# Kernel tuning notes

Hardware: AMD Instinct MI355X
Metric: run time of the kernel (lower is better)

## Reference

```python
import jax, jax.numpy as jnp
import numpy as np

D = 1024        # embedding_dim
H = 16          # num_heads
HKV = 4         # num_kv_heads
HD = D // H     # head_dim = 64
L = 64          # latent_dim
EPS = 1e-6
LN_EPS = 1e-5
B, S = 2, 1024


def _feat(x):
    # feature_map == 'elu': elu(x) + 1 (non-negative features)
    return jax.nn.elu(x) + 1.0


def setup_inputs() -> dict:
    key = jax.random.key(0)
    ks = jax.random.split(key, 8)
    w = lambda k, shape: (jax.random.normal(k, shape, jnp.float32) * 0.02)
    return {
        "x": jax.random.normal(ks[0], (B, S, D), jnp.float32),
        "Wq": w(ks[1], (D, D)), "bq": jnp.zeros((D,), jnp.float32),
        "Wk": w(ks[2], (D, HKV * HD)), "bk": jnp.zeros((HKV * HD,), jnp.float32),
        "Wv": w(ks[3], (D, HKV * HD)), "bv": jnp.zeros((HKV * HD,), jnp.float32),
        "Wc": w(ks[4], (HKV * HD, L)),   # kv_compress (no bias)
        "We": w(ks[5], (L, HKV * HD)),   # kv_expand (no bias)
        "Wo": w(ks[6], (D, D)), "bo": jnp.zeros((D,), jnp.float32),
        "gamma": jnp.ones((D,), jnp.float32),
        "beta": jnp.zeros((D,), jnp.float32),
    }


def reference(x, Wq, bq, Wk, bk, Wv, bv, Wc, We, Wo, bo, gamma, beta):
    b, s, _ = x.shape
    residual = x
    # projections
    q = x @ Wq + bq                     # [b,s,D]
    k = x @ Wk + bk                     # [b,s,HKV*HD]
    v = x @ Wv + bv
    # latent compress -> expand
    k = (k @ Wc) @ We                   # [b,s,HKV*HD]
    v = (v @ Wc) @ We
    # split heads
    q = q.reshape(b, s, H, HD).transpose(0, 2, 1, 3)      # [b,H,s,HD]
    k = k.reshape(b, s, HKV, HD).transpose(0, 2, 1, 3)    # [b,HKV,s,HD]
    v = v.reshape(b, s, HKV, HD).transpose(0, 2, 1, 3)
    # GQA: repeat KV heads per query group
    rep = H // HKV
    k = jnp.repeat(k, rep, axis=1)                        # [b,H,s,HD]
    v = jnp.repeat(v, rep, axis=1)
    # causal linear attention via cumulative KV outer-product state
    qf = _feat(q)                                          # [b,h,s,f]
    kf = _feat(k)
    kv = jnp.einsum('bhsf,bhsd->bhsfd', kf, v)             # [b,h,s,f,d]
    kv_cum = jnp.cumsum(kv, axis=2)
    num = jnp.einsum('bhsf,bhsfd->bhsd', qf, kv_cum)
    den = jnp.einsum('bhsf,bhsf->bhs', qf, jnp.cumsum(kf, axis=2))[..., None] + EPS
    o = num / den                                          # [b,h,s,d]
    # merge heads, output projection
    o = o.transpose(0, 2, 1, 3).reshape(b, s, D)
    o = o @ Wo + bo
    # residual + layernorm (epsilon=1e-5)
    y = residual + o
    mu = jnp.mean(y, axis=-1, keepdims=True)
    var = jnp.var(y, axis=-1, keepdims=True)
    return (y - mu) / jnp.sqrt(var + LN_EPS) * gamma + beta
```

## Files before the change

### kernel.cpp

```cpp
#include <hip/hip_runtime.h>

#define D_ 1024
#define H_ 16
#define HKV_ 4
#define B_ 2
#define S_ 1024
#define BS_ (B_*S_)
#define QKVW 1536
#define QB 64
#define NC (S_/QB)

typedef short bf8 __attribute__((ext_vector_type(8)));
typedef float f32x4 __attribute__((ext_vector_type(4)));

#define MFMA_B16(a,b,c) __builtin_amdgcn_mfma_f32_16x16x32_bf16((a),(b),(c),0,0,0)

#define GLOAD16(g, l) __builtin_amdgcn_global_load_lds( \
    (const __attribute__((address_space(1))) void*)(g), \
    (__attribute__((address_space(3))) void*)(l), 16, 0, 0)

#define SW(row, idx) ((idx) ^ (((row) & 7) << 3))

__device__ __forceinline__ unsigned short f2b(float f) {
  unsigned int u = __float_as_uint(f);
  u += 0x7FFFu + ((u >> 16) & 1u);
  return (unsigned short)(u >> 16);
}
__device__ __forceinline__ float b2f(unsigned short h) {
  return __uint_as_float(((unsigned int)h) << 16);
}
__device__ __forceinline__ float feat(float x) { return x > 0.f ? x + 1.f : __expf(x); }

__device__ __forceinline__ void conv_body(const float* __restrict__ src,
                                          unsigned short* __restrict__ dst,
                                          int sub, int n4, int tid) {
  int i = sub * 256 + tid;
  if (i >= n4) return;
  float4 v = ((const float4*)src)[i];
  ushort4 o;
  o.x = f2b(v.x); o.y = f2b(v.y); o.z = f2b(v.z); o.w = f2b(v.w);
  ((ushort4*)dst)[i] = o;
}

__device__ __forceinline__ void tconv_body(const float* __restrict__ src,
                                           unsigned short* __restrict__ dst,
                                           int bx, int by, int ss, int ds,
                                           int tid, float (*tl)[65]) {
  int r0 = by * 64, c0 = bx * 64;
  int ty = tid >> 4, tx4 = (tid & 15) * 4;
#pragma unroll
  for (int rep = 0; rep < 4; ++rep) {
    int r = ty + rep * 16;
    float4 v = *(const float4*)&src[(size_t)(r0 + r) * ss + c0 + tx4];
    tl[r][tx4] = v.x; tl[r][tx4 + 1] = v.y; tl[r][tx4 + 2] = v.z; tl[r][tx4 + 3] = v.w;
  }
  __syncthreads();
#pragma unroll
  for (int rep = 0; rep < 4; ++rep) {
    int c = ty + rep * 16;
    ushort4 o;
    o.x = f2b(tl[tx4 + 0][c]); o.y = f2b(tl[tx4 + 1][c]);
    o.z = f2b(tl[tx4 + 2][c]); o.w = f2b(tl[tx4 + 3][c]);
    *(ushort4*)&dst[(size_t)(c0 + c) * ds + r0 + tx4] = o;
  }
}

__global__ __launch_bounds__(256) void k_prep(const float* __restrict__ x,
                                              const float* __restrict__ Wq,
                                              const float* __restrict__ Wo,
                                              const float* __restrict__ Wk,
                                              const float* __restrict__ Wv,
                                              const float* __restrict__ Wc,
                                              const float* __restrict__ We,
                                              unsigned short* __restrict__ xb,
                                              unsigned short* __restrict__ Wqkv_t,
                                              unsigned short* __restrict__ Wo_t,
                                              unsigned short* __restrict__ Wkv_b,
                                              unsigned short* __restrict__ Wc_b,
                                              unsigned short* __restrict__ We_t) {
  __shared__ float tl[64][65];
  int blk = blockIdx.x, tid = threadIdx.x;
  if (blk < 2048) {
    conv_body(x, xb, blk, BS_ * D_ / 4, tid);
  } else if (blk < 2304) {
    conv_body(Wk, Wkv_b, blk - 2048, 1024 * 256 / 4, tid);
  } else if (blk < 2560) {
    conv_body(Wv, Wkv_b + 1024 * 256, blk - 2304, 1024 * 256 / 4, tid);
  } else if (blk < 2816) {
    int sb = blk - 2560;
    tconv_body(Wq, Wqkv_t, sb & 15, sb >> 4, 1024, 1024, tid, tl);
  } else if (blk < 3072) {
    int sb = blk - 2816;
    tconv_body(Wo, Wo_t, sb & 15, sb >> 4, 1024, 1024, tid, tl);
  } else if (blk < 3088) {
    conv_body(Wc, Wc_b, blk - 3072, 256 * 64 / 4, tid);
  } else {
    tconv_body(We, We_t, blk - 3088, 0, 256, 64, tid, tl);
  }
}

template<int MODE>
__global__ __launch_bounds__(64) void k_gemm1(const unsigned short* __restrict__ A,
                                              const unsigned short* __restrict__ Bt,
                                              const float* __restrict__ bias,
                                              void* __restrict__ C,
                                              int N, int K) {
  __shared__ __align__(16) unsigned short As[2][64 * 32];
  __shared__ __align__(16) unsigned short Bs[2][64 * 32];
  const int lane = threadIdx.x;
  const int row0 = blockIdx.y * 64, col0 = blockIdx.x * 64;
  const int lr = lane & 15, lq = lane >> 4;
  const int sr = lane >> 2, sj = lane & 3;
  const f32x4 fzero = {0.f, 0.f, 0.f, 0.f};
  f32x4 acc[4][4];
#pragma unroll
  for (int i = 0; i < 4; ++i)
#pragma unroll
    for (int j = 0; j < 4; ++j) acc[i][j] = fzero;

#define STAGE1(pb, k0)                                                          \
  {                                                                             \
    _Pragma("unroll")                                                           \
    for (int i = 0; i < 4; ++i) {                                               \
      int r = i * 16 + sr;                                                      \
      int js = sj ^ (r & 3);                                                    \
      GLOAD16(&A[(size_t)(row0 + r) * K + (k0) + js * 8],                       \
              &As[pb][(i * 64 + lane) * 8]);                                    \
    }                                                                           \
    _Pragma("unroll")                                                           \
    for (int i = 0; i < 4; ++i) {                                               \
      int r = i * 16 + sr;                                                      \
      int js = sj ^ (r & 3);                                                    \
      GLOAD16(&Bt[(size_t)(col0 + r) * K + (k0) + js * 8],                      \
              &Bs[pb][(i * 64 + lane) * 8]);                                    \
    }                                                                           \
  }

  STAGE1(0, 0);
  int cur = 0;
  for (int k0 = 0; k0 < K; k0 += 32) {
    if (k0 + 32 < K) {
      STAGE1(cur ^ 1, k0 + 32);
      asm volatile("s_waitcnt vmcnt(8)" ::: "memory");
    } else {
      asm volatile("s_waitcnt vmcnt(0)" ::: "memory");
    }
    __builtin_amdgcn_sched_barrier(0);
    bf8 af[4], bfr[4];
#pragma unroll
    for (int mi = 0; mi < 4; ++mi) {
      int ra = mi * 16 + lr;
      af[mi] = *(const bf8*)&As[cur][ra * 32 + ((lq ^ (ra & 3)) * 8)];
    }
#pragma unroll
    for (int ni = 0; ni < 4; ++ni) {
      int rb = ni * 16 + lr;
      bfr[ni] = *(const bf8*)&Bs[cur][rb * 32 + ((lq ^ (rb & 3)) * 8)];
    }
#pragma unroll
    for (int mi = 0; mi < 4; ++mi)
#pragma unroll
      for (int ni = 0; ni < 4; ++ni)
        acc[mi][ni] = MFMA_B16(af[mi], bfr[ni], acc[mi][ni]);
    cur ^= 1;
  }
#undef STAGE1
#pragma unroll
  for (int ni = 0; ni < 4; ++ni) {
    int col = col0 + ni * 16 + lr;
    float bv = bias[col];
#pragma unroll
    for (int mi = 0; mi < 4; ++mi)
#pragma unroll
      for (int r = 0; r < 4; ++r) {
        int row = row0 + mi * 16 + lq * 4 + r;
        float v = acc[mi][ni][r] + bv;
        if (MODE == 1) {
          if (col < 1280) v = feat(v);
          ((unsigned short*)C)[(size_t)row * N + col] = f2b(v);
        } else {
          ((float*)C)[(size_t)row * N + col] = v;
        }
      }
  }
}

template<int MODE>
__global__ __launch_bounds__(128) void k_gemm(const unsigned short* __restrict__ A,
                                              const unsigned short* __restrict__ Bt,
                                              void* __restrict__ C,
                                              void* __restrict__ C2,
                                              int N, int K,
                                              const float* __restrict__ fbq,
                                              const float* __restrict__ fbk,
                                              const float* __restrict__ fbv,
                                              const float* __restrict__ fWce) {
  if (MODE == 2 && blockIdx.y == 4) {
    int t = blockIdx.x * 128 + threadIdx.x;
    if (t >= QKVW) return;
    float* biasq = (float*)C2;
    if (t < 1024) { biasq[t] = fbq[t]; return; }
    const float* b = (t < 1280) ? fbk : fbv;
    int n = (t < 1280) ? (t - 1024) : (t - 1280);
    float s = 0.f;
    for (int j = 0; j < 256; ++j) s += b[j] * fWce[j * 256 + n];
    biasq[t] = s;
    return;
  }
  __shared__ __align__(16) unsigned short As[64 * 32];
  __shared__ __align__(16) unsigned short Bs[128 * 32];
  const int tid = threadIdx.x;
  const int lane = tid & 63, wave = tid >> 6;
  const int row0 = blockIdx.y * 64, col0 = blockIdx.x * 128;
  const f32x4 fzero = {0.f, 0.f, 0.f, 0.f};
  f32x4 acc[4][4];
#pragma unroll
  for (int i = 0; i < 4; ++i)
#pragma unroll
    for (int j = 0; j < 4; ++j) acc[i][j] = fzero;
  const int lr = lane & 15, lq = lane >> 4, lk = lq * 8;
  for (int k0 = 0; k0 < K; k0 += 32) {
#pragma unroll
    for (int i = 0; i < 2; ++i) {
      int e = (tid + i * 128) * 8;
      int r = e >> 5, c = e & 31;
      GLOAD16(&A[(size_t)(row0 + r) * K + k0 + c], &As[e]);
    }
#pragma unroll
    for (int i = 0; i < 4; ++i) {
      int e = (tid + i * 128) * 8;
      int r = e >> 5, c = e & 31;
      GLOAD16(&Bt[(size_t)(col0 + r) * K + k0 + c], &Bs[e]);
    }
    __syncthreads();
    bf8 af[4], bfr[4];
#pragma unroll
    for (int mi = 0; mi < 4; ++mi)
      af[mi] = *(const bf8*)&As[(mi * 16 + lr) * 32 + lk];
#pragma unroll
    for (int ni = 0; ni < 4; ++ni)
      bfr[ni] = *(const bf8*)&Bs[(wave * 64 + ni * 16 + lr) * 32 + lk];
#pragma unroll
    for (int mi = 0; mi < 4; ++mi)
#pragma unroll
      for (int ni = 0; ni < 4; ++ni)
        acc[mi][ni] = MFMA_B16(af[mi], bfr[ni], acc[mi][ni]);
    __syncthreads();
  }
#pragma unroll
  for (int mi = 0; mi < 4; ++mi)
#pragma unroll
    for (int ni = 0; ni < 4; ++ni) {
      int col = col0 + wave * 64 + ni * 16 + lr;
#pragma unroll
      for (int r = 0; r < 4; ++r) {
        int row = row0 + mi * 16 + lq * 4 + r;
        float v = acc[mi][ni][r];
        if (MODE == 2) {
          int sec = col >> 10, cc = col & 1023;
          ((unsigned short*)C)[(size_t)(1024 + sec * 256 + row) * 1024 + cc] = f2b(v);
        } else {
          ((float*)C)[(size_t)row * 256 + col] = v;
          ((unsigned short*)C2)[(size_t)col * 256 + row] = f2b(v);
        }
      }
    }
}

__global__ __launch_bounds__(256) void k_vkv(const unsigned short* __restrict__ qkvb,
                                             unsigned short* __restrict__ vt,
                                             float* __restrict__ stc) {
  __shared__ unsigned short tl[64][72];
  __shared__ float Kf[64 * 64];
  int c = blockIdx.x, g = blockIdx.y, b = blockIdx.z;
  int tid = threadIdx.x;
  int s0 = c * QB;
  {
    int j = tid >> 2, f0 = (tid & 3) * 16;
    const unsigned short* kr = &qkvb[(size_t)(b * S_ + s0 + j) * QKVW + 1024 + g * 64 + f0];
    const unsigned short* vr = &qkvb[(size_t)(b * S_ + s0 + j) * QKVW + 1280 + g * 64 + f0];
    uint4 k0_ = *(const uint4*)kr;
    uint4 k1_ = *(const uint4*)(kr + 8);
    const unsigned short* ks = (const unsigned short*)&k0_;
#pragma unroll
    for (int e = 0; e < 8; ++e) Kf[j * 64 + f0 + e] = b2f(ks[e]);
    ks = (const unsigned short*)&k1_;
#pragma unroll
    for (int e = 0; e < 8; ++e) Kf[j * 64 + f0 + 8 + e] = b2f(ks[e]);
    *(uint4*)&tl[j][f0] = *(const uint4*)vr;
    *(uint4*)&tl[j][f0 + 8] = *(const uint4*)(vr + 8);
  }
  __syncthreads();
  {
    int ty = tid >> 4, tx4 = (tid & 15) * 4;
#pragma unroll
    for (int rep = 0; rep < 4; ++rep) {
      int d = ty + rep * 16;
      ushort4 o;
      o.x = tl[tx4 + 0][d]; o.y = tl[tx4 + 1][d];
      o.z = tl[tx4 + 2][d]; o.w = tl[tx4 + 3][d];
      *(ushort4*)&vt[((size_t)(b * HKV_ + g) * 64 + d) * S_ + s0 + tx4] = o;
    }
  }
  int d = tid >> 2, f0 = (tid & 3) * 16;
  float acc[16];
#pragma unroll
  for (int e = 0; e < 16; ++e) acc[e] = 0.f;
#pragma unroll 4
  for (int j = 0; j < QB; ++j) {
    float vv = b2f(tl[j][d]);
    const float* kfr = &Kf[j * 64 + f0];
#pragma unroll
    for (int e = 0; e < 16; ++e) acc[e] += vv * kfr[e];
  }
  size_t base = ((size_t)((b * HKV_ + g) * NC + c) * 65 + d) * 64 + f0;
#pragma unroll
  for (int e = 0; e < 16; ++e) stc[base + e] = acc[e];
  if (tid < 64) {
    float z = 0.f;
    for (int j = 0; j < QB; ++j) z += Kf[j * 64 + tid];
    stc[((size_t)((b * HKV_ + g) * NC + c) * 65 + 64) * 64 + tid] = z;
  }
}

__global__ __launch_bounds__(256) void k_scan(const float* __restrict__ stc,
                                              unsigned short* __restrict__ stp,
                                              float* __restrict__ zp) {
  int t = blockIdx.x * 256 + threadIdx.x;
  if (t >= 8 * 65 * 64) return;
  int bg = t / (65 * 64);
  int e = t - bg * (65 * 64);
  int d = e >> 6, f = e & 63;
  float run = 0.f;
#pragma unroll
  for (int c = 0; c < NC; ++c) {
    if (d < 64) stp[(size_t)(bg * NC + c) * 4096 + e] = f2b(run);
    else        zp[(bg * NC + c) * 64 + f] = run;
    run += stc[((size_t)(bg * NC + c) * 65 + d) * 64 + f];
  }
}

__global__ __launch_bounds__(512) void k_attn(const unsigned short* __restrict__ qkvb,
                                              const unsigned short* __restrict__ vt,
                                              const unsigned short* __restrict__ stp,
                                              const float* __restrict__ zp,
                                              unsigned short* __restrict__ ob) {
  __shared__ __align__(16) unsigned short Qf[2][64 * 64];
  __shared__ __align__(16) unsigned short Kf[64 * 64];
  __shared__ __align__(16) unsigned short Vl[64 * 64];
  __shared__ __align__(16) unsigned short Sl[64 * 64];
  __shared__ __align__(16) unsigned short P[2][64 * 64];
  __shared__ __align__(16) unsigned short Ol[64][144];
  __shared__ float zl[64];
  __shared__ float den[2][64];
  int c = blockIdx.x, hp = blockIdx.y, b = blockIdx.z;
  int g = hp >> 1;
  int tid = threadIdx.x, lane = tid & 63, wave = tid >> 6;
  int s0 = c * QB;
  {
    int hsel = tid >> 8, t = tid & 255;
    int j = t >> 2, f0 = (t & 3) * 16;
    const unsigned short* qr =
        &qkvb[(size_t)(b * S_ + s0 + j) * QKVW + (hp * 2 + hsel) * 64 + f0];
    *(uint4*)&Qf[hsel][SW(j, j * 64 + f0)]     = *(const uint4*)qr;
    *(uint4*)&Qf[hsel][SW(j, j * 64 + f0 + 8)] = *(const uint4*)(qr + 8);
    if (tid < 256) {
      const unsigned short* kr =
          &qkvb[(size_t)(b * S_ + s0 + j) * QKVW + 1024 + g * 64 + f0];
      *(uint4*)&Kf[SW(j, j * 64 + f0)]     = *(const uint4*)kr;
      *(uint4*)&Kf[SW(j, j * 64 + f0 + 8)] = *(const uint4*)(kr + 8);
    } else {
      const unsigned short* vbase = &vt[((size_t)(b * HKV_ + g) * 64) * S_ + s0];
#pragma unroll
      for (int i2 = 0; i2 < 2; ++i2) {
        int cc = t * 2 + i2;
        int dd = cc >> 3, col = (cc & 7) * 8;
        *(uint4*)&Vl[SW(dd, cc * 8)] = *(const uint4*)&vbase[(size_t)dd * S_ + col];
      }
    }
    const unsigned short* sbase = &stp[(size_t)((b * HKV_ + g) * NC + c) * 4096];
    { int dd = tid >> 3; *(uint4*)&Sl[SW(dd, tid * 8)] = *(const uint4*)&sbase[tid * 8]; }
    if (tid < 64) zl[tid] = zp[((b * HKV_ + g) * NC + c) * 64 + tid];
  }
  __syncthreads();
  const int lr = lane & 15, lq = lane >> 4, lk = lq * 8;
  const int hh = wave >> 2, rw = (wave & 3) * 16;
  const f32x4 fzero = {0.f, 0.f, 0.f, 0.f};
  bf8 aQ[2];
#pragma unroll
  for (int kk = 0; kk < 2; ++kk)
    aQ[kk] = *(const bf8*)&Qf[hh][SW(rw + lr, (rw + lr) * 64 + kk * 32 + lk)];
  f32x4 sc[4];
#pragma unroll
  for (int nj = 0; nj < 4; ++nj) sc[nj] = fzero;
#pragma unroll
  for (int nj = 0; nj < 4; ++nj)
#pragma unroll
    for (int kk = 0; kk < 2; ++kk) {
      bf8 bk8 = *(const bf8*)&Kf[SW(nj * 16 + lr, (nj * 16 + lr) * 64 + kk * 32 + lk)];
      sc[nj] = MFMA_B16(aQ[kk], bk8, sc[nj]);
    }
#pragma unroll
  for (int nj = 0; nj < 4; ++nj)
#pragma unroll
    for (int r = 0; r < 4; ++r) {
      int i = rw + lq * 4 + r;
      int j = nj * 16 + lr;
      float v = (j <= i) ? sc[nj][r] : 0.f;
      P[hh][SW(i, i * 64 + j)] = f2b(v);
    }
  __syncthreads();
  {
    int hd = tid >> 8, t = tid & 255;
    int i = t >> 2, q = t & 3, f0 = q * 16;
    float s = 0.f;
#pragma unroll
    for (int e = 0; e < 16; ++e) s += b2f(P[hd][SW(i, i * 64 + f0 + e)]);
#pragma unroll
    for (int e = 0; e < 16; ++e) s += b2f(Qf[hd][SW(i, i * 64 + f0 + e)]) * zl[f0 + e];
    s += __shfl_xor(s, 1);
    s += __shfl_xor(s, 2);
    if (q == 0) den[hd][i] = s;
  }
  f32x4 oa[4];
#pragma unroll
  for (int nd = 0; nd < 4; ++nd) oa[nd] = fzero;
  bf8 aP[2];
#pragma unroll
  for (int kk = 0; kk < 2; ++kk)
    aP[kk] = *(const bf8*)&P[hh][SW(rw + lr, (rw + lr) * 64 + kk * 32 + lk)];
#pragma unroll
  for (int nd = 0; nd < 4; ++nd)
#pragma unroll
    for (int kk = 0; kk < 2; ++kk) {
      bf8 bS = *(const bf8*)&Sl[SW(nd * 16 + lr, (nd * 16 + lr) * 64 + kk * 32 + lk)];
      oa[nd] = MFMA_B16(aQ[kk], bS, oa[nd]);
      bf8 bV = *(const bf8*)&Vl[SW(nd * 16 + lr, (nd * 16 + lr) * 64 + kk * 32 + lk)];
      oa[nd] = MFMA_B16(aP[kk], bV, oa[nd]);
    }
  __syncthreads();
#pragma unroll
  for (int nd = 0; nd < 4; ++nd)
#pragma unroll
    for (int r = 0; r < 4; ++r) {
      int i = rw + lq * 4 + r;
      int dd = nd * 16 + lr;
      Ol[i][hh * 64 + dd] = f2b(oa[nd][r] / (den[hh][i] + 1e-6f));
    }
  __syncthreads();
  {
    int j = tid >> 3, u = tid & 7;
    unsigned short* orow = &ob[(size_t)(b * S_ + s0 + j) * D_ + hp * 128 + u * 16];
    *(uint4*)orow       = *(const uint4*)&Ol[j][u * 16];
    *(uint4*)(orow + 8) = *(const uint4*)&Ol[j][u * 16 + 8];
  }
}

__global__ __launch_bounds__(256) void k_ln(const float* __restrict__ x,
                                            const float* __restrict__ o2,
                                            const float* __restrict__ gamma,
                                            const float* __restrict__ beta,
                                            float* __restrict__ out) {
  int row = blockIdx.x, tid = threadIdx.x;
  float4 xv = ((const float4*)(x + (size_t)row * D_))[tid];
  float4 ov = ((const float4*)(o2 + (size_t)row * D_))[tid];
  float4 y;
  y.x = xv.x + ov.x; y.y = xv.y + ov.y; y.z = xv.z + ov.z; y.w = xv.w + ov.w;
  float s = y.x + y.y + y.z + y.w;
  float ss = y.x * y.x + y.y * y.y + y.z * y.z + y.w * y.w;
#pragma unroll
  for (int off = 32; off > 0; off >>= 1) {
    s += __shfl_down(s, off);
    ss += __shfl_down(ss, off);
  }
  __shared__ float red[8];
  int lane = tid & 63, wave = tid >> 6;
  if (lane == 0) { red[wave] = s; red[4 + wave] = ss; }
  __syncthreads();
  if (tid == 0) {
    red[0] = red[0] + red[1] + red[2] + red[3];
    red[4] = red[4] + red[5] + red[6] + red[7];
  }
  __syncthreads();
  float mu = red[0] * (1.f / D_);
  float var = red[4] * (1.f / D_) - mu * mu;
  float rs = rsqrtf(var + 1e-5f);
  float4 g4 = ((const float4*)gamma)[tid];
  float4 b4 = ((const float4*)beta)[tid];
  float4 o;
  o.x = (y.x - mu) * rs * g4.x + b4.x;
  o.y = (y.y - mu) * rs * g4.y + b4.y;
  o.z = (y.z - mu) * rs * g4.z + b4.z;
  o.w = (y.w - mu) * rs * g4.w + b4.w;
  ((float4*)(out + (size_t)row * D_))[tid] = o;
}

extern "C" void kernel_launch(void* const* d_in, const int* in_sizes, int n_in,
                              void* d_out, int out_size, void* d_ws, size_t ws_size,
                              hipStream_t stream) {
  const float* x     = (const float*)d_in[0];
  const float* Wq    = (const float*)d_in[1];
  const float* bq    = (const float*)d_in[2];
  const float* Wk    = (const float*)d_in[3];
  const float* bk    = (const float*)d_in[4];
  const float* Wv    = (const float*)d_in[5];
  const float* bv    = (const float*)d_in[6];
  const float* Wc    = (const float*)d_in[7];
  const float* We    = (const float*)d_in[8];
  const float* Wo    = (const float*)d_in[9];
  const float* bo    = (const float*)d_in[10];
  const float* gamma = (const float*)d_in[11];
  const float* beta  = (const float*)d_in[12];

  char* p = (char*)d_ws;
  size_t off = 0;
  auto carve = [&](size_t bytes) {
    void* r = p + off;
    off = (off + bytes + 255) & ~(size_t)255;
    return r;
  };
  unsigned short* xb     = (unsigned short*)carve((size_t)BS_ * D_ * 2);
  unsigned short* Wqkv_t = (unsigned short*)carve((size_t)QKVW * D_ * 2);
  unsigned short* Wo_t   = (unsigned short*)carve((size_t)D_ * D_ * 2);
  float*          biasq  = (float*)carve(QKVW * 4);
  unsigned short* qkvb   = (unsigned short*)carve((size_t)BS_ * QKVW * 2);
  unsigned short* Wc_b   = (unsigned short*)carve(256 * 64 * 2);
  unsigned short* We_t   = (unsigned short*)carve(256 * 64 * 2);
  float*          Wce    = (float*)carve(256 * 256 * 4);
  unsigned short* Wce_t  = (unsigned short*)carve(256 * 256 * 2);
  unsigned short* Wkv_b  = (unsigned short*)carve((size_t)2048 * 256 * 2);
  unsigned short* vtb    = (unsigned short*)carve((size_t)8 * 64 * S_ * 2);
  float*          stc    = (float*)carve((size_t)8 * NC * 65 * 64 * 4);
  unsigned short* stp    = (unsigned short*)carve((size_t)8 * NC * 4096 * 2);
  float*          zp     = (float*)carve((size_t)8 * NC * 64 * 4);
  unsigned short* obuf   = (unsigned short*)carve((size_t)BS_ * D_ * 2);
  float*          o2     = (float*)carve((size_t)BS_ * D_ * 4);

  k_prep<<<3092, 256, 0, stream>>>(x, Wq, Wo, Wk, Wv, Wc, We,
                                   xb, Wqkv_t, Wo_t, Wkv_b, Wc_b, We_t);
  k_gemm<3><<<dim3(2, 4), 128, 0, stream>>>(Wc_b, We_t, Wce, Wce_t,
                                            256, 64, nullptr, nullptr, nullptr, nullptr);
  k_gemm<2><<<dim3(16, 5), 128, 0, stream>>>(Wce_t, Wkv_b, Wqkv_t, biasq,
                                             2048, 256, bq, bk, bv, Wce);
  k_gemm1<1><<<dim3(24, 32), 64, 0, stream>>>(xb, Wqkv_t, biasq, qkvb, QKVW, 1024);
  k_vkv<<<dim3(NC, HKV_, B_), 256, 0, stream>>>(qkvb, vtb, stc);
  k_scan<<<(8 * 65 * 64 + 255) / 256, 256, 0, stream>>>(stc, stp, zp);
  k_attn<<<dim3(NC, H_ / 2, B_), 512, 0, stream>>>(qkvb, vtb, stp, zp, obuf);
  k_gemm1<0><<<dim3(16, 32), 64, 0, stream>>>(obuf, Wo_t, bo, o2, 1024, 1024);
  k_ln<<<BS_, 256, 0, stream>>>(x, o2, gamma, beta, (float*)d_out);
}
```

Baseline: 97.50 us.

## Fuse Wc·We fold into prep, deepen GEMM K-tile, store output projection and residual in bf16

```diff
diff --git a/kernel.cpp b/kernel.cpp
--- a/kernel.cpp
+++ b/kernel.cpp
@@ -76,9 +76,11 @@
                                               unsigned short* __restrict__ Wqkv_t,
                                               unsigned short* __restrict__ Wo_t,
                                               unsigned short* __restrict__ Wkv_b,
-                                              unsigned short* __restrict__ Wc_b,
-                                              unsigned short* __restrict__ We_t) {
+                                              float* __restrict__ Wce,
+                                              unsigned short* __restrict__ Wce_t) {
   __shared__ float tl[64][65];
+  __shared__ __align__(16) unsigned short As[64][72];
+  __shared__ __align__(16) unsigned short Bs[128][72];
   int blk = blockIdx.x, tid = threadIdx.x;
   if (blk < 2048) {
     conv_body(x, xb, blk, BS_ * D_ / 4, tid);
@@ -92,10 +94,59 @@
   } else if (blk < 3072) {
     int sb = blk - 2816;
     tconv_body(Wo, Wo_t, sb & 15, sb >> 4, 1024, 1024, tid, tl);
-  } else if (blk < 3088) {
-    conv_body(Wc, Wc_b, blk - 3072, 256 * 64 / 4, tid);
   } else {
-    tconv_body(We, We_t, blk - 3088, 0, 256, 64, tid, tl);
+    int sb = blk - 3072;
+    int row0 = (sb >> 1) * 64, col0 = (sb & 1) * 128;
+    {
+      int r = tid >> 2, c0 = (tid & 3) * 16;
+      const float* src = &Wc[(size_t)(row0 + r) * 64 + c0];
+#pragma unroll
+      for (int e = 0; e < 16; e += 4) {
+        float4 v = *(const float4*)(src + e);
+        As[r][c0 + e] = f2b(v.x); As[r][c0 + e + 1] = f2b(v.y);
+        As[r][c0 + e + 2] = f2b(v.z); As[r][c0 + e + 3] = f2b(v.w);
+      }
+      int k = tid >> 2, cb = (tid & 3) * 32;
+      const float* wsrc = &We[(size_t)k * 256 + col0 + cb];
+#pragma unroll
+      for (int e = 0; e < 32; e += 4) {
+        float4 v = *(const float4*)(wsrc + e);
+        Bs[cb + e][k] = f2b(v.x); Bs[cb + e + 1][k] = f2b(v.y);
+        Bs[cb + e + 2][k] = f2b(v.z); Bs[cb + e + 3][k] = f2b(v.w);
+      }
+    }
+    __syncthreads();
+    const int lane = tid & 63, wave = tid >> 6;
+    const int lr = lane & 15, lq = lane >> 4;
+    const int wc0 = wave * 32;
+    const f32x4 fzero = {0.f, 0.f, 0.f, 0.f};
+    f32x4 acc[4][2];
+#pragma unroll
+    for (int i = 0; i < 4; ++i) { acc[i][0] = fzero; acc[i][1] = fzero; }
+#pragma unroll
+    for (int kk = 0; kk < 2; ++kk)
+#pragma unroll
+      for (int mi = 0; mi < 4; ++mi) {
+        bf8 a = *(const bf8*)&As[mi * 16 + lr][kk * 32 + lq * 8];
+#pragma unroll
+        for (int ni = 0; ni < 2; ++ni) {
+          bf8 bb = *(const bf8*)&Bs[wc0 + ni * 16 + lr][kk * 32 + lq * 8];
+          acc[mi][ni] = MFMA_B16(a, bb, acc[mi][ni]);
+        }
+      }
+#pragma unroll
+    for (int mi = 0; mi < 4; ++mi)
+#pragma unroll
+      for (int ni = 0; ni < 2; ++ni) {
+        int col = col0 + wc0 + ni * 16 + lr;
+#pragma unroll
+        for (int r = 0; r < 4; ++r) {
+          int row = row0 + mi * 16 + lq * 4 + r;
+          float v = acc[mi][ni][r];
+          Wce[(size_t)row * 256 + col] = v;
+          Wce_t[(size_t)col * 256 + row] = f2b(v);
+        }
+      }
   }
 }
 
@@ -103,14 +154,15 @@
 __global__ __launch_bounds__(64) void k_gemm1(const unsigned short* __restrict__ A,
                                               const unsigned short* __restrict__ Bt,
                                               const float* __restrict__ bias,
-                                              void* __restrict__ C,
+                                              unsigned short* __restrict__ C,
                                               int N, int K) {
-  __shared__ __align__(16) unsigned short As[2][64 * 32];
-  __shared__ __align__(16) unsigned short Bs[2][64 * 32];
+  __shared__ __align__(16) unsigned short As[2][64 * 64];
+  __shared__ __align__(16) unsigned short Bs[2][64 * 64];
   const int lane = threadIdx.x;
   const int row0 = blockIdx.y * 64, col0 = blockIdx.x * 64;
   const int lr = lane & 15, lq = lane >> 4;
-  const int sr = lane >> 2, sj = lane & 3;
+  const int rsub = lane >> 3, sj = lane & 7;
+  const int js = sj ^ rsub;
   const f32x4 fzero = {0.f, 0.f, 0.f, 0.f};
   f32x4 acc[4][4];
 #pragma unroll
@@ -118,53 +170,47 @@
 #pragma unroll
     for (int j = 0; j < 4; ++j) acc[i][j] = fzero;
 
-#define STAGE1(pb, k0)                                                          \
-  {                                                                             \
-    _Pragma("unroll")                                                           \
-    for (int i = 0; i < 4; ++i) {                                               \
-      int r = i * 16 + sr;                                                      \
-      int js = sj ^ (r & 3);                                                    \
-      GLOAD16(&A[(size_t)(row0 + r) * K + (k0) + js * 8],                       \
-              &As[pb][(i * 64 + lane) * 8]);                                    \
-    }                                                                           \
-    _Pragma("unroll")                                                           \
-    for (int i = 0; i < 4; ++i) {                                               \
-      int r = i * 16 + sr;                                                      \
-      int js = sj ^ (r & 3);                                                    \
-      GLOAD16(&Bt[(size_t)(col0 + r) * K + (k0) + js * 8],                      \
-              &Bs[pb][(i * 64 + lane) * 8]);                                    \
-    }                                                                           \
-  }
-
-  STAGE1(0, 0);
+#define STAGE64(pb, k0)                                                        \
+  {                                                                            \
+    _Pragma("unroll")                                                          \
+    for (int i = 0; i < 8; ++i)                                                \
+      GLOAD16(&A[(size_t)(row0 + i * 8 + rsub) * K + (k0) + js * 8],           \
+              &As[pb][(i * 512 + lane * 8)]);                                  \
+    _Pragma("unroll")                                                          \
+    for (int i = 0; i < 8; ++i)                                                \
+      GLOAD16(&Bt[(size_t)(col0 + i * 8 + rsub) * K + (k0) + js * 8],          \
+              &Bs[pb][(i * 512 + lane * 8)]);                                  \
+  }
+
+  STAGE64(0, 0);
   int cur = 0;
-  for (int k0 = 0; k0 < K; k0 += 32) {
-    if (k0 + 32 < K) {
-      STAGE1(cur ^ 1, k0 + 32);
-      asm volatile("s_waitcnt vmcnt(8)" ::: "memory");
+  for (int k0 = 0; k0 < K; k0 += 64) {
+    if (k0 + 64 < K) {
+      STAGE64(cur ^ 1, k0 + 64);
+      asm volatile("s_waitcnt vmcnt(16)" ::: "memory");
     } else {
       asm volatile("s_waitcnt vmcnt(0)" ::: "memory");
     }
     __builtin_amdgcn_sched_barrier(0);
-    bf8 af[4], bfr[4];
-#pragma unroll
-    for (int mi = 0; mi < 4; ++mi) {
-      int ra = mi * 16 + lr;
-      af[mi] = *(const bf8*)&As[cur][ra * 32 + ((lq ^ (ra & 3)) * 8)];
-    }
-#pragma unroll
-    for (int ni = 0; ni < 4; ++ni) {
-      int rb = ni * 16 + lr;
-      bfr[ni] = *(const bf8*)&Bs[cur][rb * 32 + ((lq ^ (rb & 3)) * 8)];
-    }
-#pragma unroll
-    for (int mi = 0; mi < 4; ++mi)
-#pragma unroll
-      for (int ni = 0; ni < 4; ++ni)
-        acc[mi][ni] = MFMA_B16(af[mi], bfr[ni], acc[mi][ni]);
+    bf8 af[2][4], bfr[2][4];
+#pragma unroll
+    for (int kk = 0; kk < 2; ++kk)
+#pragma unroll
+      for (int mi = 0; mi < 4; ++mi) {
+        int ch = (kk * 4 + lq) ^ (lr & 7);
+        af[kk][mi]  = *(const bf8*)&As[cur][(mi * 16 + lr) * 64 + ch * 8];
+        bfr[kk][mi] = *(const bf8*)&Bs[cur][(mi * 16 + lr) * 64 + ch * 8];
+      }
+#pragma unroll
+    for (int kk = 0; kk < 2; ++kk)
+#pragma unroll
+      for (int mi = 0; mi < 4; ++mi)
+#pragma unroll
+        for (int ni = 0; ni < 4; ++ni)
+          acc[mi][ni] = MFMA_B16(af[kk][mi], bfr[kk][ni], acc[mi][ni]);
     cur ^= 1;
   }
-#undef STAGE1
+#undef STAGE64
 #pragma unroll
   for (int ni = 0; ni < 4; ++ni) {
     int col = col0 + ni * 16 + lr;
@@ -175,30 +221,24 @@
       for (int r = 0; r < 4; ++r) {
         int row = row0 + mi * 16 + lq * 4 + r;
         float v = acc[mi][ni][r] + bv;
-        if (MODE == 1) {
-          if (col < 1280) v = feat(v);
-          ((unsigned short*)C)[(size_t)row * N + col] = f2b(v);
-        } else {
-          ((float*)C)[(size_t)row * N + col] = v;
-        }
-      }
-  }
-}
-
-template<int MODE>
-__global__ __launch_bounds__(128) void k_gemm(const unsigned short* __restrict__ A,
+        if (MODE == 1 && col < 1280) v = feat(v);
+        C[(size_t)row * N + col] = f2b(v);
+      }
+  }
+}
+
+__global__ __launch_bounds__(128) void k_fold(const unsigned short* __restrict__ A,
                                               const unsigned short* __restrict__ Bt,
-                                              void* __restrict__ C,
-                                              void* __restrict__ C2,
+                                              unsigned short* __restrict__ C,
+                                              float* __restrict__ biasq,
                                               int N, int K,
                                               const float* __restrict__ fbq,
                                               const float* __restrict__ fbk,
                                               const float* __restrict__ fbv,
                                               const float* __restrict__ fWce) {
-  if (MODE == 2 && blockIdx.y == 4) {
+  if (blockIdx.y == 4) {
     int t = blockIdx.x * 128 + threadIdx.x;
     if (t >= QKVW) return;
-    float* biasq = (float*)C2;
     if (t < 1024) { biasq[t] = fbq[t]; return; }
     const float* b = (t < 1280) ? fbk : fbv;
     int n = (t < 1280) ? (t - 1024) : (t - 1280);
@@ -255,14 +295,8 @@
 #pragma unroll
       for (int r = 0; r < 4; ++r) {
         int row = row0 + mi * 16 + lq * 4 + r;
-        float v = acc[mi][ni][r];
-        if (MODE == 2) {
-          int sec = col >> 10, cc = col & 1023;
-          ((unsigned short*)C)[(size_t)(1024 + sec * 256 + row) * 1024 + cc] = f2b(v);
-        } else {
-          ((float*)C)[(size_t)row * 256 + col] = v;
-          ((unsigned short*)C2)[(size_t)col * 256 + row] = f2b(v);
-        }
+        int sec = col >> 10, cc = col & 1023;
+        C[(size_t)(1024 + sec * 256 + row) * 1024 + cc] = f2b(acc[mi][ni][r]);
       }
     }
 }
@@ -456,16 +490,17 @@
   }
 }
 
-__global__ __launch_bounds__(256) void k_ln(const float* __restrict__ x,
-                                            const float* __restrict__ o2,
+__global__ __launch_bounds__(256) void k_ln(const unsigned short* __restrict__ xb,
+                                            const unsigned short* __restrict__ o2,
                                             const float* __restrict__ gamma,
                                             const float* __restrict__ beta,
                                             float* __restrict__ out) {
   int row = blockIdx.x, tid = threadIdx.x;
-  float4 xv = ((const float4*)(x + (size_t)row * D_))[tid];
-  float4 ov = ((const float4*)(o2 + (size_t)row * D_))[tid];
+  ushort4 xv = ((const ushort4*)(xb + (size_t)row * D_))[tid];
+  ushort4 ov = ((const ushort4*)(o2 + (size_t)row * D_))[tid];
   float4 y;
-  y.x = xv.x + ov.x; y.y = xv.y + ov.y; y.z = xv.z + ov.z; y.w = xv.w + ov.w;
+  y.x = b2f(xv.x) + b2f(ov.x); y.y = b2f(xv.y) + b2f(ov.y);
+  y.z = b2f(xv.z) + b2f(ov.z); y.w = b2f(xv.w) + b2f(ov.w);
   float s = y.x + y.y + y.z + y.w;
   float ss = y.x * y.x + y.y * y.y + y.z * y.z + y.w * y.w;
 #pragma unroll
@@ -524,8 +559,6 @@
   unsigned short* Wo_t   = (unsigned short*)carve((size_t)D_ * D_ * 2);
   float*          biasq  = (float*)carve(QKVW * 4);
   unsigned short* qkvb   = (unsigned short*)carve((size_t)BS_ * QKVW * 2);
-  unsigned short* Wc_b   = (unsigned short*)carve(256 * 64 * 2);
-  unsigned short* We_t   = (unsigned short*)carve(256 * 64 * 2);
   float*          Wce    = (float*)carve(256 * 256 * 4);
   unsigned short* Wce_t  = (unsigned short*)carve(256 * 256 * 2);
   unsigned short* Wkv_b  = (unsigned short*)carve((size_t)2048 * 256 * 2);
@@ -534,18 +567,16 @@
   unsigned short* stp    = (unsigned short*)carve((size_t)8 * NC * 4096 * 2);
   float*          zp     = (float*)carve((size_t)8 * NC * 64 * 4);
   unsigned short* obuf   = (unsigned short*)carve((size_t)BS_ * D_ * 2);
-  float*          o2     = (float*)carve((size_t)BS_ * D_ * 4);
-
-  k_prep<<<3092, 256, 0, stream>>>(x, Wq, Wo, Wk, Wv, Wc, We,
-                                   xb, Wqkv_t, Wo_t, Wkv_b, Wc_b, We_t);
-  k_gemm<3><<<dim3(2, 4), 128, 0, stream>>>(Wc_b, We_t, Wce, Wce_t,
-                                            256, 64, nullptr, nullptr, nullptr, nullptr);
-  k_gemm<2><<<dim3(16, 5), 128, 0, stream>>>(Wce_t, Wkv_b, Wqkv_t, biasq,
-                                             2048, 256, bq, bk, bv, Wce);
+  unsigned short* o2     = (unsigned short*)carve((size_t)BS_ * D_ * 2);
+
+  k_prep<<<3080, 256, 0, stream>>>(x, Wq, Wo, Wk, Wv, Wc, We,
+                                   xb, Wqkv_t, Wo_t, Wkv_b, Wce, Wce_t);
+  k_fold<<<dim3(16, 5), 128, 0, stream>>>(Wce_t, Wkv_b, Wqkv_t, biasq,
+                                          2048, 256, bq, bk, bv, Wce);
   k_gemm1<1><<<dim3(24, 32), 64, 0, stream>>>(xb, Wqkv_t, biasq, qkvb, QKVW, 1024);
   k_vkv<<<dim3(NC, HKV_, B_), 256, 0, stream>>>(qkvb, vtb, stc);
   k_scan<<<(8 * 65 * 64 + 255) / 256, 256, 0, stream>>>(stc, stp, zp);
   k_attn<<<dim3(NC, H_ / 2, B_), 512, 0, stream>>>(qkvb, vtb, stp, zp, obuf);
   k_gemm1<0><<<dim3(16, 32), 64, 0, stream>>>(obuf, Wo_t, bo, o2, 1024, 1024);
-  k_ln<<<BS_, 256, 0, stream>>>(x, o2, gamma, beta, (float*)d_out);
-}
+  k_ln<<<BS_, 256, 0, stream>>>(xb, o2, gamma, beta, (float*)d_out);
+}
```

Result: faster. 90.92 us (-6.8%).
